# Kernel tuning notes

Hardware: AMD Instinct MI355X
Metric: run time of the kernel (lower is better)

The kernel has to match this reference:

```python
import jax, jax.numpy as jnp
import numpy as np

SCALE = np.array([90.0, 180.0], dtype=np.float32)  # lat, long scaling
FILL = 2.0  # sentinel distance for masked-out locations


def setup_inputs() -> dict:
    key = jax.random.key(0)
    k1, k2, k3 = jax.random.split(key, 3)
    B, S, L = 1024, 128, 256  # batch, samples_per_qa, max_locs
    question_latlongs = jax.random.uniform(k1, (B, L, 2), dtype=jnp.float32, minval=-1.0, maxval=1.0)
    question_latlong_mask = jax.random.randint(k2, (B, L), 0, 2).astype(jnp.bool_)
    entity_latlongs = jax.random.uniform(k3, (B, S, 2), dtype=jnp.float32, minval=-1.0, maxval=1.0)
    return {
        "question_latlongs": question_latlongs,
        "question_latlong_mask": question_latlong_mask,
        "entity_latlongs": entity_latlongs,
    }


def reference(question_latlongs, question_latlong_mask, entity_latlongs):
    # question_latlongs: [B, L, 2], mask: [B, L] bool, entity_latlongs: [B, S, 2]
    scale = jnp.asarray(SCALE, dtype=question_latlongs.dtype)
    q = jnp.deg2rad(question_latlongs * scale)  # [B, L, 2]
    c = jnp.deg2rad(entity_latlongs * scale)    # [B, S, 2]
    # haversine distance between every entity sample and every question loc
    dlat = q[:, None, :, 0] - c[:, :, None, 0]  # [B, S, L]
    dlon = q[:, None, :, 1] - c[:, :, None, 1]  # [B, S, L]
    a = jnp.sin(dlat / 2) ** 2 + (
        jnp.cos(c[:, :, None, 0]) * jnp.cos(q[:, None, :, 0]) * jnp.sin(dlon / 2) ** 2
    )  # [B, S, L]
    dis = jnp.arcsin(jnp.sqrt(a))
    # masked locations get sentinel 2.0 (also covers all-False rows, which the
    # torch loop skips leaving dist == 2)
    dist = jnp.where(question_latlong_mask[:, None, :], dis, FILL)
    min_x = -jnp.min(dist, axis=-1)[..., None]  # [B, S, 1]
    return min_x
```

## Files before the change

kernel.cpp:

```cpp
#include <hip/hip_runtime.h>

#define NB 1024
#define NS 128
#define NL 256

__global__ __launch_bounds__(256) void distance_encoder_kernel(
    const float* __restrict__ q,
    const unsigned char* __restrict__ mraw,
    const float* __restrict__ ent,
    float* __restrict__ out)
{
    __shared__ float4       s_q[NL];
    __shared__ unsigned int s_mrow[NL/4];
    __shared__ float        s_part[NS];
    __shared__ int          s_u8;

    const int b   = blockIdx.x;
    const int tid = threadIdx.x;

    const float2 ql = reinterpret_cast<const float2*>(q)[b * NL + tid];
    const int    s  = tid & (NS - 1);
    const float2 el = reinterpret_cast<const float2*>(ent)[b * NS + s];

    if (tid < 64) {
        const unsigned int w =
            reinterpret_cast<const unsigned int*>(mraw)[b * (NL / 4) + tid];
        s_mrow[tid] = w;
        const bool nz = (w & 0xFFFFFF00u) != 0;
        const unsigned long long bal = __ballot(nz);
        if (tid == 0) s_u8 = (bal != 0ull) ? 1 : 0;
    }
    __syncthreads();

    {
        float sl, cl, so, co;
        sincosf(ql.x * 1.5707963267948966f, &sl, &cl);
        sincosf(ql.y * 3.1415926535897932f, &so, &co);
        int mk;
        if (s_u8) {
            mk = (s_mrow[tid >> 2] >> ((tid & 3) * 8)) & 0xFF;
        } else {
            mk = reinterpret_cast<const int*>(mraw)[b * NL + tid];
        }
        s_q[tid] = make_float4(sl, cl * so, cl * co, mk ? 0.5f : 1.0e9f);
    }

    float sle, cle, soe, coe;
    sincosf(el.x * 1.5707963267948966f, &sle, &cle);
    sincosf(el.y * 3.1415926535897932f, &soe, &coe);
    const float k1 = -0.5f * sle;
    const float k2 = -0.5f * cle * soe;
    const float k3 = -0.5f * cle * coe;

    __syncthreads();

    const int half = tid >> 7;
    const int l0   = half * (NL / 2);
    float amin0 = 1.0e30f, amin1 = 1.0e30f;
    #pragma unroll 8
    for (int i = 0; i < NL / 2; i += 2) {
        const float4 qa = s_q[l0 + i];
        const float4 qb = s_q[l0 + i + 1];
        float a0 = fmaf(k1, qa.x, qa.w);
        a0 = fmaf(k2, qa.y, a0);
        a0 = fmaf(k3, qa.z, a0);
        float a1 = fmaf(k1, qb.x, qb.w);
        a1 = fmaf(k2, qb.y, a1);
        a1 = fmaf(k3, qb.z, a1);
        amin0 = fminf(amin0, a0);
        amin1 = fminf(amin1, a1);
    }
    float amin = fminf(amin0, amin1);

    if (half == 0) s_part[s] = amin;
    __syncthreads();
    if (half == 1) {
        amin = fminf(amin, s_part[s]);
        const float dis = (amin > 1.0e8f)
                        ? 2.0f
                        : asinf(sqrtf(fminf(fmaxf(amin, 0.0f), 1.0f)));
        out[b * NS + s] = -dis;
    }
}

extern "C" void kernel_launch(void* const* d_in, const int* in_sizes, int n_in,
                              void* d_out, int out_size, void* d_ws, size_t ws_size,
                              hipStream_t stream) {
    const float* q            = (const float*)d_in[0];
    const unsigned char* mraw = (const unsigned char*)d_in[1];
    const float* ent          = (const float*)d_in[2];
    float* out                = (float*)d_out;

    distance_encoder_kernel<<<NB, 256, 0, stream>>>(q, mraw, ent, out);
}
```

Baseline: 11.53 us.

## Register-tile 4 samples per thread and use hardware sin/cos intrinsics

Each thread now computes four entity samples against a 32-location chunk, so every float4 loaded from LDS is reused across four samples instead of one. Entity coefficients are computed once by the first 128 threads and staged in shared memory, and the eight chunk partial minima are reduced at the end. sincosf is replaced with __builtin_amdgcn_sinf/cosf on inputs prescaled into revolutions, which removes the software range reduction. The hardware trig has lower accuracy, and the extra sync and reduction add some overhead.

```diff
diff --git a/kernel.cpp b/kernel.cpp
--- a/kernel.cpp
+++ b/kernel.cpp
@@ -11,75 +11,87 @@
     float* __restrict__ out)
 {
     __shared__ float4       s_q[NL];
+    __shared__ float4       s_k[NS];
+    __shared__ float        s_part[8][NS];
     __shared__ unsigned int s_mrow[NL/4];
-    __shared__ float        s_part[NS];
     __shared__ int          s_u8;
 
-    const int b   = blockIdx.x;
-    const int tid = threadIdx.x;
+    const int b    = blockIdx.x;
+    const int tid  = threadIdx.x;
+    const int lane = tid & 63;
+    const int w    = tid >> 6;
+    const int lh   = lane >> 5;
+    const int sb   = lane & 31;
+    const int chunk = w * 2 + lh;
 
     const float2 ql = reinterpret_cast<const float2*>(q)[b * NL + tid];
-    const int    s  = tid & (NS - 1);
-    const float2 el = reinterpret_cast<const float2*>(ent)[b * NS + s];
+    float2 el;
+    if (tid < NS) el = reinterpret_cast<const float2*>(ent)[b * NS + tid];
 
     if (tid < 64) {
-        const unsigned int w =
+        const unsigned int wd =
             reinterpret_cast<const unsigned int*>(mraw)[b * (NL / 4) + tid];
-        s_mrow[tid] = w;
-        const bool nz = (w & 0xFFFFFF00u) != 0;
-        const unsigned long long bal = __ballot(nz);
+        s_mrow[tid] = wd;
+        const unsigned long long bal = __ballot((wd & 0xFFFFFF00u) != 0);
         if (tid == 0) s_u8 = (bal != 0ull) ? 1 : 0;
     }
     __syncthreads();
 
     {
-        float sl, cl, so, co;
-        sincosf(ql.x * 1.5707963267948966f, &sl, &cl);
-        sincosf(ql.y * 3.1415926535897932f, &so, &co);
+        const float sl = __builtin_amdgcn_sinf(ql.x * 0.25f);
+        const float cl = __builtin_amdgcn_cosf(ql.x * 0.25f);
+        const float so = __builtin_amdgcn_sinf(ql.y * 0.5f);
+        const float co = __builtin_amdgcn_cosf(ql.y * 0.5f);
         int mk;
-        if (s_u8) {
-            mk = (s_mrow[tid >> 2] >> ((tid & 3) * 8)) & 0xFF;
-        } else {
-            mk = reinterpret_cast<const int*>(mraw)[b * NL + tid];
-        }
+        if (s_u8) mk = (s_mrow[tid >> 2] >> ((tid & 3) * 8)) & 0xFF;
+        else      mk = reinterpret_cast<const int*>(mraw)[b * NL + tid];
         s_q[tid] = make_float4(sl, cl * so, cl * co, mk ? 0.5f : 1.0e9f);
     }
-
-    float sle, cle, soe, coe;
-    sincosf(el.x * 1.5707963267948966f, &sle, &cle);
-    sincosf(el.y * 3.1415926535897932f, &soe, &coe);
-    const float k1 = -0.5f * sle;
-    const float k2 = -0.5f * cle * soe;
-    const float k3 = -0.5f * cle * coe;
-
+    if (tid < NS) {
+        const float sle = __builtin_amdgcn_sinf(el.x * 0.25f);
+        const float cle = __builtin_amdgcn_cosf(el.x * 0.25f);
+        const float soe = __builtin_amdgcn_sinf(el.y * 0.5f);
+        const float coe = __builtin_amdgcn_cosf(el.y * 0.5f);
+        s_k[tid] = make_float4(-0.5f * sle, -0.5f * cle * soe,
+                               -0.5f * cle * coe, 0.0f);
+    }
     __syncthreads();
 
-    const int half = tid >> 7;
-    const int l0   = half * (NL / 2);
-    float amin0 = 1.0e30f, amin1 = 1.0e30f;
+    const float4 k0 = s_k[sb];
+    const float4 k1 = s_k[sb + 32];
+    const float4 k2 = s_k[sb + 64];
+    const float4 k3 = s_k[sb + 96];
+
+    float m0 = 1e30f, m1 = 1e30f, m2 = 1e30f, m3 = 1e30f;
+    const int l0 = chunk * 32;
     #pragma unroll 8
-    for (int i = 0; i < NL / 2; i += 2) {
-        const float4 qa = s_q[l0 + i];
-        const float4 qb = s_q[l0 + i + 1];
-        float a0 = fmaf(k1, qa.x, qa.w);
-        a0 = fmaf(k2, qa.y, a0);
-        a0 = fmaf(k3, qa.z, a0);
-        float a1 = fmaf(k1, qb.x, qb.w);
-        a1 = fmaf(k2, qb.y, a1);
-        a1 = fmaf(k3, qb.z, a1);
-        amin0 = fminf(amin0, a0);
-        amin1 = fminf(amin1, a1);
+    for (int i = 0; i < 32; ++i) {
+        const float4 qq = s_q[l0 + i];
+        float a0 = fmaf(k0.x, qq.x, qq.w);
+        float a1 = fmaf(k1.x, qq.x, qq.w);
+        float a2 = fmaf(k2.x, qq.x, qq.w);
+        float a3 = fmaf(k3.x, qq.x, qq.w);
+        a0 = fmaf(k0.y, qq.y, a0);  a0 = fmaf(k0.z, qq.z, a0);
+        a1 = fmaf(k1.y, qq.y, a1);  a1 = fmaf(k1.z, qq.z, a1);
+        a2 = fmaf(k2.y, qq.y, a2);  a2 = fmaf(k2.z, qq.z, a2);
+        a3 = fmaf(k3.y, qq.y, a3);  a3 = fmaf(k3.z, qq.z, a3);
+        m0 = fminf(m0, a0);  m1 = fminf(m1, a1);
+        m2 = fminf(m2, a2);  m3 = fminf(m3, a3);
     }
-    float amin = fminf(amin0, amin1);
+    s_part[chunk][sb]      = m0;
+    s_part[chunk][sb + 32] = m1;
+    s_part[chunk][sb + 64] = m2;
+    s_part[chunk][sb + 96] = m3;
+    __syncthreads();
 
-    if (half == 0) s_part[s] = amin;
-    __syncthreads();
-    if (half == 1) {
-        amin = fminf(amin, s_part[s]);
-        const float dis = (amin > 1.0e8f)
+    if (tid < NS) {
+        float mm = s_part[0][tid];
+        #pragma unroll
+        for (int c = 1; c < 8; ++c) mm = fminf(mm, s_part[c][tid]);
+        const float dis = (mm > 1.0e8f)
                         ? 2.0f
-                        : asinf(sqrtf(fminf(fmaxf(amin, 0.0f), 1.0f)));
-        out[b * NS + s] = -dis;
+                        : asinf(sqrtf(fminf(fmaxf(mm, 0.0f), 1.0f)));
+        out[b * NS + tid] = -dis;
     }
 }
 
```

Result: faster. 10.43 us (-9.5%).
